# Kernel optimization log

Hardware: AMD Instinct MI355X
Metric: run time of the kernel (lower is better)

The kernel has to match this reference:

```python
import jax, jax.numpy as jnp
import numpy as np

S, B, H = 2048, 2, 1024
NH = 16
HD = H // NH
EPS = 1e-5


def _ln(z, w, b):
    m = jnp.mean(z, axis=-1, keepdims=True)
    v = jnp.mean(jnp.square(z - m), axis=-1, keepdims=True)
    return (z - m) * jax.lax.rsqrt(v + EPS) * w + b


def setup_inputs() -> dict:
    key = jax.random.key(0)
    ks = jax.random.split(key, 8)
    std = 0.02
    return {
        "x": jax.random.normal(ks[0], (S, B, H), dtype=jnp.float32),
        "ln1_w": jnp.ones((H,), jnp.float32),
        "ln1_b": jnp.zeros((H,), jnp.float32),
        "w_qkv": jax.random.normal(ks[1], (3 * H, H), jnp.float32) * std,
        "b_qkv": jnp.zeros((3 * H,), jnp.float32),
        "w_proj": jax.random.normal(ks[2], (H, H), jnp.float32) * std,
        "b_proj": jnp.zeros((H,), jnp.float32),
        "ln2_w": jnp.ones((H,), jnp.float32),
        "ln2_b": jnp.zeros((H,), jnp.float32),
        "w_fc1": jax.random.normal(ks[3], (4 * H, H), jnp.float32) * std,
        "b_fc1": jnp.zeros((4 * H,), jnp.float32),
        "w_fc2": jax.random.normal(ks[4], (H, 4 * H), jnp.float32) * std,
        "b_fc2": jnp.zeros((H,), jnp.float32),
    }


def reference(x, ln1_w, ln1_b, w_qkv, b_qkv, w_proj, b_proj,
              ln2_w, ln2_b, w_fc1, b_fc1, w_fc2, b_fc2):
    s, b, h = x.shape
    # --- LayerNormLinear: LN then fused QKV projection ---
    residual = x
    qkv = _ln(x, ln1_w, ln1_b) @ w_qkv.T + b_qkv            # [S, B, 3H]
    # per-head interleaved packing: [S, B, NH, 3*HD] then split on last dim
    qkv = qkv.reshape(s, b, NH, 3 * HD).transpose(1, 2, 0, 3)  # [B, NH, S, 3HD]
    q, k, v = jnp.split(qkv, 3, axis=3)                      # each [B, NH, S, HD]
    # --- naive causal attention with full SxS scores ---
    scores = jnp.einsum("bhsd,bhtd->bhst", q, k) * (HD ** -0.5)
    causal = jnp.triu(jnp.ones((s, s), dtype=bool), k=1)
    scores = jnp.where(causal, -jnp.inf, scores)
    attn = jax.nn.softmax(scores, axis=-1)                   # [B, NH, S, S]
    out = jnp.einsum("bhst,bhtd->bhsd", attn, v)             # [B, NH, S, HD]
    out = out.transpose(0, 2, 1, 3).reshape(b, s, h).transpose(1, 0, 2)  # [S, B, H]
    out = out @ w_proj.T + b_proj
    x = residual + out
    # --- LayerNormMLP: LN -> fc1 -> gelu(tanh) -> fc2, residual ---
    residual = x
    hmid = jax.nn.gelu(_ln(x, ln2_w, ln2_b) @ w_fc1.T + b_fc1, approximate=True)
    x = residual + (hmid @ w_fc2.T + b_fc2)
    return x
```

## Files before the change

### kernel.cpp

```cpp
#include <hip/hip_runtime.h>
#include <math.h>

#define S_LEN 2048
#define B_SZ 2
#define NHEAD 16
#define HDIM 64
#define H_DIM 1024
#define M_ROWS (S_LEN * B_SZ)
#define LN_EPS 1e-5f
#define KSTR 72
#define SCL 0.18033688011112042f

typedef __attribute__((ext_vector_type(4))) float f32x4;
typedef __attribute__((ext_vector_type(8))) short short8;
typedef __attribute__((ext_vector_type(8))) unsigned short u16x8;
typedef __attribute__((ext_vector_type(4))) unsigned short u16x4;
typedef __attribute__((ext_vector_type(2))) unsigned short u16x2;

__device__ __forceinline__ float bf2f(unsigned short u) {
    return __uint_as_float(((unsigned int)u) << 16);
}
__device__ __forceinline__ unsigned short f2bf(float f) {
    unsigned int u = __float_as_uint(f);
    return (unsigned short)((u + 0x7fffu + ((u >> 16) & 1u)) >> 16);
}

__global__ __launch_bounds__(256) void cast_all(const float* __restrict__ wqkv,
                                                const float* __restrict__ wproj,
                                                const float* __restrict__ wfc1,
                                                const float* __restrict__ wfc2,
                                                unsigned short* __restrict__ oqkv,
                                                unsigned short* __restrict__ oproj,
                                                unsigned short* __restrict__ ofc1,
                                                unsigned short* __restrict__ ofc2) {
    const int i = blockIdx.x * 256 + threadIdx.x;
    const float* src; unsigned short* dst; int off;
    if (i < 786432)       { src = wqkv;  dst = oqkv;  off = i; }
    else if (i < 1048576) { src = wproj; dst = oproj; off = i - 786432; }
    else if (i < 2097152) { src = wfc1;  dst = ofc1;  off = i - 1048576; }
    else                  { src = wfc2;  dst = ofc2;  off = i - 2097152; }
    f32x4 v = ((const f32x4*)src)[off];
    u16x4 o;
    o.x = f2bf(v.x); o.y = f2bf(v.y); o.z = f2bf(v.z); o.w = f2bf(v.w);
    ((u16x4*)dst)[off] = o;
}

__global__ __launch_bounds__(256) void ln_bf16(const float* __restrict__ x,
                                               const float* __restrict__ w,
                                               const float* __restrict__ b,
                                               unsigned short* __restrict__ y) {
    const int m = blockIdx.x;
    const int tid = threadIdx.x;
    const float* row = x + (size_t)m * H_DIM;

    float4 v = ((const float4*)row)[tid];
    float s  = v.x + v.y + v.z + v.w;
    float ss = v.x * v.x + v.y * v.y + v.z * v.z + v.w * v.w;

    __shared__ float rs[4], rss[4], stats[2];
    const int wave = tid >> 6, lane = tid & 63;
    for (int off = 32; off; off >>= 1) {
        s  += __shfl_down(s, off);
        ss += __shfl_down(ss, off);
    }
    if (lane == 0) { rs[wave] = s; rss[wave] = ss; }
    __syncthreads();
    if (tid == 0) {
        float S = rs[0] + rs[1] + rs[2] + rs[3];
        float SS = rss[0] + rss[1] + rss[2] + rss[3];
        float mean = S * (1.0f / H_DIM);
        float var = SS * (1.0f / H_DIM) - mean * mean;
        stats[0] = mean;
        stats[1] = rsqrtf(var + LN_EPS);
    }
    __syncthreads();
    const float mean = stats[0], inv = stats[1];
    float4 wv = ((const float4*)w)[tid];
    float4 bv = ((const float4*)b)[tid];
    u16x4 o;
    o.x = f2bf((v.x - mean) * inv * wv.x + bv.x);
    o.y = f2bf((v.y - mean) * inv * wv.y + bv.y);
    o.z = f2bf((v.z - mean) * inv * wv.z + bv.z);
    o.w = f2bf((v.w - mean) * inv * wv.w + bv.w);
    ((u16x4*)(y + (size_t)m * H_DIM))[tid] = o;
}

template <int EPI, bool BF_OUT, int TN>
__global__ __launch_bounds__(256) void gemm_mfma(const unsigned short* __restrict__ A,
                                                 const unsigned short* __restrict__ B,
                                                 const float* __restrict__ bias,
                                                 const float* __restrict__ resid,
                                                 void* __restrict__ Cout,
                                                 int M, int N, int K) {
    constexpr int NJ = TN / 32;
    constexpr int ST = 72;
    constexpr int BNR = (TN == 128) ? 4 : 2;
    __shared__ __attribute__((aligned(16))) unsigned short As[128 * ST];
    __shared__ __attribute__((aligned(16))) unsigned short Bs[TN * ST];

    const int tid = threadIdx.x;
    const int wid = tid >> 6;
    const int ln  = tid & 63;
    const int quad = ln >> 4;
    const int mr   = ln & 15;
    const int wm = (wid >> 1) * 64;
    const int wn = (wid & 1) * (TN / 2);

    const int mb = M >> 7;
    const int stripe = mb >> 3;
    const int xcd = blockIdx.x & 7;
    const int local = blockIdx.x >> 3;
    const int m0 = (xcd * stripe + (local % stripe)) << 7;
    const int n0 = (local / stripe) * TN;

    const int ar = tid >> 1, aks = (tid & 1) * 32;
    const unsigned short* gA = A + (size_t)(m0 + ar) * K + aks;
    unsigned short* lA = As + ar * ST + aks;
    const int br  = (TN == 128) ? (tid >> 1) : (tid >> 2);
    const int bks = (TN == 128) ? ((tid & 1) * 32) : ((tid & 3) * 16);
    const unsigned short* gB = B + (size_t)(n0 + br) * K + bks;
    unsigned short* lB = Bs + br * ST + bks;

    u16x8 apf[4], bpf[BNR];
    auto load_tile = [&](int kt) {
        const unsigned short* pa = gA + kt * 64;
#pragma unroll
        for (int r = 0; r < 4; r++) apf[r] = *(const u16x8*)(pa + r * 8);
        const unsigned short* pb = gB + kt * 64;
#pragma unroll
        for (int r = 0; r < BNR; r++) bpf[r] = *(const u16x8*)(pb + r * 8);
    };
    auto store_tile = [&]() {
#pragma unroll
        for (int r = 0; r < 4; r++) *(u16x8*)(lA + r * 8) = apf[r];
#pragma unroll
        for (int r = 0; r < BNR; r++) *(u16x8*)(lB + r * 8) = bpf[r];
    };

    const f32x4 zero = {0.f, 0.f, 0.f, 0.f};
    f32x4 acc[4][NJ];
#pragma unroll
    for (int i = 0; i < 4; i++)
#pragma unroll
        for (int j = 0; j < NJ; j++) acc[i][j] = zero;

    const int nt = K >> 6;
    load_tile(0);
    store_tile();
    if (nt > 1) load_tile(1);
    __syncthreads();

    for (int kt = 0; kt < nt; kt++) {
#pragma unroll
        for (int h = 0; h < 2; h++) {
            short8 af[4], bf[NJ];
#pragma unroll
            for (int i = 0; i < 4; i++)
                af[i] = *(const short8*)(As + (wm + i * 16 + mr) * ST + h * 32 + quad * 8);
#pragma unroll
            for (int j = 0; j < NJ; j++)
                bf[j] = *(const short8*)(Bs + (wn + j * 16 + mr) * ST + h * 32 + quad * 8);
#pragma unroll
            for (int i = 0; i < 4; i++)
#pragma unroll
                for (int j = 0; j < NJ; j++)
                    acc[i][j] = __builtin_amdgcn_mfma_f32_16x16x32_bf16(bf[j], af[i], acc[i][j], 0, 0, 0);
        }
        if (kt + 1 < nt) {
            __syncthreads();
            store_tile();
            if (kt + 2 < nt) load_tile(kt + 2);
            __syncthreads();
        }
    }

    f32x4 bias4[NJ];
#pragma unroll
    for (int j = 0; j < NJ; j++)
        bias4[j] = *(const f32x4*)(bias + n0 + wn + j * 16 + quad * 4);

#pragma unroll
    for (int i = 0; i < 4; i++) {
        const int m = m0 + wm + i * 16 + mr;
#pragma unroll
        for (int j = 0; j < NJ; j++) {
            const int nb = n0 + wn + j * 16 + quad * 4;
            f32x4 v = acc[i][j] + bias4[j];
            if (EPI == 1) v += *(const f32x4*)(resid + (size_t)m * N + nb);
            if (EPI == 2) {
#pragma unroll
                for (int r = 0; r < 4; r++) {
                    const float t = v[r];
                    v[r] = 0.5f * t * (1.0f + tanhf(0.7978845608f * (t + 0.044715f * t * t * t)));
                }
            }
            if (BF_OUT) {
                u16x4 pk;
                pk.x = f2bf(v.x); pk.y = f2bf(v.y); pk.z = f2bf(v.z); pk.w = f2bf(v.w);
                *(u16x4*)((unsigned short*)Cout + (size_t)m * N + nb) = pk;
            } else {
                *(f32x4*)((float*)Cout + (size_t)m * N + nb) = v;
            }
        }
    }
}

__global__ __launch_bounds__(256) void attn_mfma(const unsigned short* __restrict__ qkv,
                                                 unsigned short* __restrict__ out) {
    __shared__ __attribute__((aligned(16))) unsigned short Ks[64 * KSTR];
    __shared__ __attribute__((aligned(16))) unsigned short Vs[64 * KSTR];
    __shared__ __attribute__((aligned(16))) unsigned short Ps[64 * KSTR];

    const int tid = threadIdx.x;
    const int wid = tid >> 6;
    const int ln  = tid & 63;
    const int quad = ln >> 4;
    const int mr   = ln & 15;

    const int id = blockIdx.x;
    const int local = id >> 3;
    const int bh = (id & 7) * 4 + (local >> 4);
    const int pa = local & 15;
    const int b  = bh >> 4;
    const int nh = bh & 15;
    const size_t chan = (size_t)nh * 192;

    const int ksr = tid >> 2, ksc = tid & 3;
    const int vt0 = (tid & 31) * 2, vd0 = (tid >> 5) * 8;

    u16x8 kp0, kp1, vp0, vp1;

#pragma unroll
    for (int half = 0; half < 2; half++) {
        const int qt = half ? (31 - pa) : pa;
        const int qb = qt * 64;

        short8 qf0, qf1;
        {
            const int qrow = qb + wid * 16 + mr;
            const unsigned short* gq = qkv + ((size_t)(qrow * 2 + b)) * 3072 + chan + quad * 8;
            qf0 = *(const short8*)gq;
            qf1 = *(const short8*)(gq + 32);
        }

        const f32x4 zero = {0.f, 0.f, 0.f, 0.f};
        f32x4 o[4];
        float ps = 0.f;
#pragma unroll
        for (int d = 0; d < 4; d++) o[d] = zero;

        {
            const unsigned short* gk = qkv + ((size_t)(ksr * 2 + b)) * 3072 + chan + 64 + ksc * 16;
            kp0 = *(const u16x8*)gk;
            kp1 = *(const u16x8*)(gk + 8);
            const unsigned short* gv = qkv + ((size_t)(vt0 * 2 + b)) * 3072 + chan + 128 + vd0;
            vp0 = *(const u16x8*)gv;
            vp1 = *(const u16x8*)(gv + 6144);
        }

        for (int kt = 0; kt <= qt; kt++) {
            __syncthreads();
            *(u16x8*)(Ks + ksr * KSTR + ksc * 16) = kp0;
            *(u16x8*)(Ks + ksr * KSTR + ksc * 16 + 8) = kp1;
#pragma unroll
            for (int j = 0; j < 8; j++) {
                u16x2 pr; pr.x = vp0[j]; pr.y = vp1[j];
                *(u16x2*)(Vs + (vd0 + j) * KSTR + vt0) = pr;
            }
            if (kt < qt) {
                const int nb = (kt + 1) * 64;
                const unsigned short* gk =
                    qkv + ((size_t)((nb + ksr) * 2 + b)) * 3072 + chan + 64 + ksc * 16;
                kp0 = *(const u16x8*)gk;
                kp1 = *(const u16x8*)(gk + 8);
                const unsigned short* gv =
                    qkv + ((size_t)((nb + vt0) * 2 + b)) * 3072 + chan + 128 + vd0;
                vp0 = *(const u16x8*)gv;
                vp1 = *(const u16x8*)(gv + 6144);
            }
            __syncthreads();

            f32x4 sacc[4];
#pragma unroll
            for (int n = 0; n < 4; n++) {
                sacc[n] = zero;
                const unsigned short* kb = Ks + (n * 16 + mr) * KSTR + quad * 8;
                short8 kfr0 = *(const short8*)kb;
                short8 kfr1 = *(const short8*)(kb + 32);
                sacc[n] = __builtin_amdgcn_mfma_f32_16x16x32_bf16(kfr0, qf0, sacc[n], 0, 0, 0);
                sacc[n] = __builtin_amdgcn_mfma_f32_16x16x32_bf16(kfr1, qf1, sacc[n], 0, 0, 0);
            }
            if (kt == qt) {
#pragma unroll
                for (int n = 0; n < 4; n++)
#pragma unroll
                    for (int r = 0; r < 4; r++)
                        if (n * 16 + quad * 4 + r > wid * 16 + mr) sacc[n][r] = -3.0e38f;
            }

            unsigned short* prow = Ps + (wid * 16 + mr) * KSTR + quad * 4;
#pragma unroll
            for (int n = 0; n < 4; n++) {
                u16x4 pk;
#pragma unroll
                for (int r = 0; r < 4; r++) {
                    const float p = exp2f(fminf(sacc[n][r] * SCL, 80.f));
                    ps += p;
                    pk[r] = (unsigned short)(__float_as_uint(p) >> 16);
                }
                *(u16x4*)(prow + n * 16) = pk;
            }

            {
                const unsigned short* pb = Ps + (wid * 16 + mr) * KSTR + quad * 8;
                short8 pa0 = *(const short8*)pb;
                short8 pa1 = *(const short8*)(pb + 32);
#pragma unroll
                for (int d = 0; d < 4; d++) {
                    const unsigned short* vb = Vs + (d * 16 + mr) * KSTR + quad * 8;
                    short8 vf0 = *(const short8*)vb;
                    short8 vf1 = *(const short8*)(vb + 32);
                    o[d] = __builtin_amdgcn_mfma_f32_16x16x32_bf16(vf0, pa0, o[d], 0, 0, 0);
                    o[d] = __builtin_amdgcn_mfma_f32_16x16x32_bf16(vf1, pa1, o[d], 0, 0, 0);
                }
            }
        }

        ps += __shfl_xor(ps, 16);
        ps += __shfl_xor(ps, 32);
        const float inv = 1.0f / ps;
        const int qrow = qb + wid * 16 + mr;
        unsigned short* po = out + ((size_t)(qrow * 2 + b)) * H_DIM + nh * HDIM;
#pragma unroll
        for (int d = 0; d < 4; d++) {
            u16x4 pk;
#pragma unroll
            for (int r = 0; r < 4; r++) pk[r] = f2bf(o[d][r] * inv);
            *(u16x4*)(po + d * 16 + quad * 4) = pk;
        }
    }
}

extern "C" void kernel_launch(void* const* d_in, const int* in_sizes, int n_in,
                              void* d_out, int out_size, void* d_ws, size_t ws_size,
                              hipStream_t stream) {
    const float* x      = (const float*)d_in[0];
    const float* ln1_w  = (const float*)d_in[1];
    const float* ln1_b  = (const float*)d_in[2];
    const float* w_qkv  = (const float*)d_in[3];
    const float* b_qkv  = (const float*)d_in[4];
    const float* w_proj = (const float*)d_in[5];
    const float* b_proj = (const float*)d_in[6];
    const float* ln2_w  = (const float*)d_in[7];
    const float* ln2_b  = (const float*)d_in[8];
    const float* w_fc1  = (const float*)d_in[9];
    const float* b_fc1  = (const float*)d_in[10];
    const float* w_fc2  = (const float*)d_in[11];
    const float* b_fc2  = (const float*)d_in[12];
    float* out = (float*)d_out;

    char* ws = (char*)d_ws;
    unsigned short* wqkv_bf  = (unsigned short*)(ws);
    unsigned short* wproj_bf = (unsigned short*)(ws + ((size_t)6 << 20));
    unsigned short* wfc1_bf  = (unsigned short*)(ws + ((size_t)8 << 20));
    unsigned short* wfc2_bf  = (unsigned short*)(ws + ((size_t)16 << 20));
    unsigned short* ln_buf   = (unsigned short*)(ws + ((size_t)24 << 20));
    unsigned short* qkv_bf   = (unsigned short*)(ws + ((size_t)32 << 20));
    unsigned short* attn_bf  = (unsigned short*)(ws + ((size_t)56 << 20));
    unsigned short* fc1_bf   = (unsigned short*)(ws + ((size_t)32 << 20));

    cast_all<<<12288, 256, 0, stream>>>(w_qkv, w_proj, w_fc1, w_fc2,
                                        wqkv_bf, wproj_bf, wfc1_bf, wfc2_bf);

    ln_bf16<<<M_ROWS, 256, 0, stream>>>(x, ln1_w, ln1_b, ln_buf);
    gemm_mfma<0, true, 128><<<768, 256, 0, stream>>>(
        ln_buf, wqkv_bf, b_qkv, nullptr, qkv_bf, M_ROWS, 3072, 1024);
    attn_mfma<<<512, 256, 0, stream>>>(qkv_bf, attn_bf);
    gemm_mfma<1, false, 64><<<512, 256, 0, stream>>>(
        attn_bf, wproj_bf, b_proj, x, out, M_ROWS, 1024, 1024);
    ln_bf16<<<M_ROWS, 256, 0, stream>>>(out, ln2_w, ln2_b, ln_buf);
    gemm_mfma<2, true, 128><<<1024, 256, 0, stream>>>(
        ln_buf, wfc1_bf, b_fc1, nullptr, fc1_bf, M_ROWS, 4096, 1024);
    gemm_mfma<1, false, 64><<<512, 256, 0, stream>>>(
        fc1_bf, wfc2_bf, b_fc2, out, out, M_ROWS, 1024, 4096);
}
```

Before: 355.7 us.

## Load GEMM tiles directly to LDS with XOR swizzle and cheaper GELU

The GEMM now uses global_load_lds to copy A and B tiles straight from global memory into LDS, skipping the register round-trip. It replaces the padded LDS stride with an XOR-swizzled unpadded layout to avoid bank conflicts. The old register prefetch of the next tile is removed, so the load for tile kt+1 is issued after compute finishes and must land before the next barrier; with a single buffer there is little overlap between loads and compute. The GELU epilogue also replaces tanhf with an exp2-based sigmoid identity, which is cheaper.

```diff
diff --git a/kernel.cpp b/kernel.cpp
--- a/kernel.cpp
+++ b/kernel.cpp
@@ -16,6 +16,9 @@
 typedef __attribute__((ext_vector_type(8))) unsigned short u16x8;
 typedef __attribute__((ext_vector_type(4))) unsigned short u16x4;
 typedef __attribute__((ext_vector_type(2))) unsigned short u16x2;
+
+typedef __attribute__((address_space(3))) unsigned int lds_u32;
+typedef const __attribute__((address_space(1))) unsigned int glb_u32;
 
 __device__ __forceinline__ float bf2f(unsigned short u) {
     return __uint_as_float(((unsigned int)u) << 16);
@@ -92,11 +95,11 @@
                                                  const float* __restrict__ resid,
                                                  void* __restrict__ Cout,
                                                  int M, int N, int K) {
-    constexpr int NJ = TN / 32;
-    constexpr int ST = 72;
-    constexpr int BNR = (TN == 128) ? 4 : 2;
-    __shared__ __attribute__((aligned(16))) unsigned short As[128 * ST];
-    __shared__ __attribute__((aligned(16))) unsigned short Bs[TN * ST];
+    constexpr int NJ  = TN / 32;
+    constexpr int ANI = 4;
+    constexpr int BNI = TN / 32;
+    __shared__ __attribute__((aligned(16))) unsigned short As[128 * 64];
+    __shared__ __attribute__((aligned(16))) unsigned short Bs[TN * 64];
 
     const int tid = threadIdx.x;
     const int wid = tid >> 6;
@@ -113,28 +116,27 @@
     const int m0 = (xcd * stripe + (local % stripe)) << 7;
     const int n0 = (local / stripe) * TN;
 
-    const int ar = tid >> 1, aks = (tid & 1) * 32;
-    const unsigned short* gA = A + (size_t)(m0 + ar) * K + aks;
-    unsigned short* lA = As + ar * ST + aks;
-    const int br  = (TN == 128) ? (tid >> 1) : (tid >> 2);
-    const int bks = (TN == 128) ? ((tid & 1) * 32) : ((tid & 3) * 16);
-    const unsigned short* gB = B + (size_t)(n0 + br) * K + bks;
-    unsigned short* lB = Bs + br * ST + bks;
-
-    u16x8 apf[4], bpf[BNR];
-    auto load_tile = [&](int kt) {
-        const unsigned short* pa = gA + kt * 64;
-#pragma unroll
-        for (int r = 0; r < 4; r++) apf[r] = *(const u16x8*)(pa + r * 8);
-        const unsigned short* pb = gB + kt * 64;
-#pragma unroll
-        for (int r = 0; r < BNR; r++) bpf[r] = *(const u16x8*)(pb + r * 8);
-    };
-    auto store_tile = [&]() {
-#pragma unroll
-        for (int r = 0; r < 4; r++) *(u16x8*)(lA + r * 8) = apf[r];
-#pragma unroll
-        for (int r = 0; r < BNR; r++) *(u16x8*)(lB + r * 8) = bpf[r];
+    const int lr = ln >> 3, lc = ln & 7;
+    const size_t Kb = (size_t)K * 2;
+    const char* gA = (const char*)A + (size_t)(m0 + wid * 32 + lr) * Kb
+                     + (size_t)((lc << 4) ^ (lr << 4));
+    const int bwr = (TN == 128) ? wid * 32 : wid * 16;
+    const char* gB = (const char*)B + (size_t)(n0 + bwr + lr) * Kb
+                     + (size_t)((lc << 4) ^ (lr << 4));
+    unsigned int* lA = (unsigned int*)As + wid * (ANI * 256);
+    unsigned int* lB = (unsigned int*)Bs + wid * (BNI * 256);
+
+    auto stage = [&](int kt) {
+        const char* pa = gA + (size_t)kt * 128;
+#pragma unroll
+        for (int i = 0; i < ANI; i++)
+            __builtin_amdgcn_global_load_lds((glb_u32*)(pa + (size_t)i * 8 * Kb),
+                                             (lds_u32*)(lA + i * 256), 16, 0, 0);
+        const char* pb = gB + (size_t)kt * 128;
+#pragma unroll
+        for (int i = 0; i < BNI; i++)
+            __builtin_amdgcn_global_load_lds((glb_u32*)(pb + (size_t)i * 8 * Kb),
+                                             (lds_u32*)(lB + i * 256), 16, 0, 0);
     };
 
     const f32x4 zero = {0.f, 0.f, 0.f, 0.f};
@@ -145,21 +147,22 @@
         for (int j = 0; j < NJ; j++) acc[i][j] = zero;
 
     const int nt = K >> 6;
-    load_tile(0);
-    store_tile();
-    if (nt > 1) load_tile(1);
-    __syncthreads();
-
+    stage(0);
+
+    const int swz = (mr & 7) << 3;
     for (int kt = 0; kt < nt; kt++) {
+        __syncthreads();
 #pragma unroll
         for (int h = 0; h < 2; h++) {
             short8 af[4], bf[NJ];
 #pragma unroll
             for (int i = 0; i < 4; i++)
-                af[i] = *(const short8*)(As + (wm + i * 16 + mr) * ST + h * 32 + quad * 8);
+                af[i] = *(const short8*)(As + (wm + i * 16 + mr) * 64
+                                            + ((h * 32 + quad * 8) ^ swz));
 #pragma unroll
             for (int j = 0; j < NJ; j++)
-                bf[j] = *(const short8*)(Bs + (wn + j * 16 + mr) * ST + h * 32 + quad * 8);
+                bf[j] = *(const short8*)(Bs + (wn + j * 16 + mr) * 64
+                                            + ((h * 32 + quad * 8) ^ swz));
 #pragma unroll
             for (int i = 0; i < 4; i++)
 #pragma unroll
@@ -168,9 +171,7 @@
         }
         if (kt + 1 < nt) {
             __syncthreads();
-            store_tile();
-            if (kt + 2 < nt) load_tile(kt + 2);
-            __syncthreads();
+            stage(kt + 1);
         }
     }
 
@@ -191,7 +192,9 @@
 #pragma unroll
                 for (int r = 0; r < 4; r++) {
                     const float t = v[r];
-                    v[r] = 0.5f * t * (1.0f + tanhf(0.7978845608f * (t + 0.044715f * t * t * t)));
+                    const float u = t + 0.044715f * t * t * t;
+                    const float e = exp2f(2.3022112f * u);
+                    v[r] = t - t / (e + 1.0f);
                 }
             }
             if (BF_OUT) {
```

Result: no change. 350.4 us (-1.5%).
